# Kernel tuning notes

Measured on AMD Instinct MI355X. Metric: run time of the kernel, lower is better.

The kernel has to match this reference:

```python
import jax, jax.numpy as jnp
import numpy as np

B, N, H, NH, P = 32, 400, 512, 8, 3
DK = H // NH
SCALE = DK ** -0.5
EPS = 1e-5


def _ln(x, g, b):
    m = jnp.mean(x, axis=-1, keepdims=True)
    v = jnp.mean((x - m) ** 2, axis=-1, keepdims=True)
    return (x - m) * jax.lax.rsqrt(v + EPS) * g + b


def _split(x):  # [B,N,H] -> [B,h,N,dk]
    return x.reshape(x.shape[0], x.shape[1], NH, DK).transpose(0, 2, 1, 3)


def _merge(x):  # [B,h,N,dk] -> [B,N,H]
    return x.transpose(0, 2, 1, 3).reshape(x.shape[0], x.shape[2], H)


def _attn(q, k, v, mask):
    s = jnp.einsum('bhid,bhjd->bhij', q, k) * SCALE
    s = s * (1.0 + mask[:, None])  # learned multiplicative prior mask
    p = jax.nn.softmax(s, axis=-1)
    return jnp.einsum('bhij,bhjd->bhid', p, v)


def _weight_gen(pri, z, C, wq, keys, wf, bf):
    # pooled token query attends over the num_priors prior matrices
    qv = jnp.mean(z @ wq, axis=1)  # [B,H]
    aw = jax.nn.softmax((qv @ keys.T) * (H ** -0.5), axis=-1)  # [B,P]
    w = jnp.einsum('bp,bpij->bij', aw, pri)  # [B,N,N] fused prior mask
    fused = jnp.einsum('bij,bjh->bih', C, z) @ wf + bf  # [B,N,H] neighborhood fusion
    return w, aw, fused


def _ffn(x, w1, b1, w2, b2):
    return jax.nn.gelu(x @ w1 + b1, approximate=False) @ w2 + b2


def _forward(x_FC, x_SC, pri_FC, pri_SC, FC, SC, dw,
             ln_attn_FC_g, ln_attn_FC_b, ln_attn_SC_g, ln_attn_SC_b,
             ln_ffn_FC_g, ln_ffn_FC_b, ln_ffn_SC_g, ln_ffn_SC_b,
             qkv_FC_w, qkv_SC_w,
             ffn_FC_w1, ffn_FC_b1, ffn_FC_w2, ffn_FC_b2,
             ffn_SC_w1, ffn_SC_b1, ffn_SC_w2, ffn_SC_b2,
             wg_q_w, wg_keys, wg_fuse_w, wg_fuse_b,
             dist_in_FC_w, dist_in_FC_b, dist_in_SC_w, dist_in_SC_b,
             dist_out_FC_w, dist_out_FC_b, dist_out_SC_w, dist_out_SC_b):
    z_FC = _ln(x_FC, ln_attn_FC_g, ln_attn_FC_b)
    z_SC = _ln(x_SC, ln_attn_SC_g, ln_attn_SC_b)
    q_FC, k_FC, v_FC = [_split(t) for t in jnp.split(z_FC @ qkv_FC_w, 3, axis=-1)]
    q_SC, k_SC, v_SC = [_split(t) for t in jnp.split(z_SC @ qkv_SC_w, 3, axis=-1)]
    w_FC, aw_FC, fused_FC = _weight_gen(pri_FC, z_FC, FC, wg_q_w, wg_keys, wg_fuse_w, wg_fuse_b)
    w_SC, aw_SC, fused_SC = _weight_gen(pri_SC, z_SC, SC, wg_q_w, wg_keys, wg_fuse_w, wg_fuse_b)
    ctx_FC = _merge(_attn(q_FC, k_FC, v_FC, w_FC))
    ctx_SC = _merge(_attn(q_SC, k_SC, v_SC, w_SC))
    attn_out_FC = x_FC + ctx_FC + fused_FC
    attn_out_SC = x_SC + ctx_SC + fused_SC
    x_FC_new = attn_out_FC + _ffn(_ln(attn_out_FC, ln_ffn_FC_g, ln_ffn_FC_b), ffn_FC_w1, ffn_FC_b1, ffn_FC_w2, ffn_FC_b2)
    x_SC_new = attn_out_SC + _ffn(_ln(attn_out_SC, ln_ffn_SC_g, ln_ffn_SC_b), ffn_SC_w1, ffn_SC_b1, ffn_SC_w2, ffn_SC_b2)
    wf, ws = dw[0], dw[1]
    proj_FC = x_FC_new @ dist_in_FC_w + dist_in_FC_b
    proj_SC = x_SC_new @ dist_in_SC_w + dist_in_SC_b
    l_FC = jax.nn.log_softmax(proj_FC.reshape(-1, H), axis=-1)
    l_SC = jax.nn.log_softmax(proj_SC.reshape(-1, H), axis=-1)
    p_FC = jnp.exp(l_FC)
    p_SC = jnp.exp(l_SC)
    rows = jnp.float32(l_FC.shape[0])
    kl_FC = jnp.sum(p_SC * (l_SC - l_FC)) / rows  # KLDiv(batchmean)(l_FC, p_SC)
    kl_SC = jnp.sum(p_FC * (l_FC - l_SC)) / rows
    x_FC_out = (1.0 - wf) * x_FC_new + wf * (proj_FC @ dist_out_FC_w + dist_out_FC_b)
    x_SC_out = (1.0 - ws) * x_SC_new + ws * (proj_SC @ dist_out_SC_w + dist_out_SC_b)
    distill_loss = 0.5 * (kl_FC * wf + kl_SC * ws)
    return (x_FC_out, x_SC_out, distill_loss, aw_FC, aw_SC)


def setup_inputs() -> dict:
    key = jax.random.key(0)
    ks = jax.random.split(key, 24)
    init = lambda k, shape: 0.02 * jax.random.normal(k, shape, jnp.float32)
    d = {}
    d['x_FC'] = jax.random.normal(ks[0], (B, N, H), jnp.float32)
    d['x_SC'] = jax.random.normal(ks[1], (B, N, H), jnp.float32)
    d['pri_FC'] = jax.random.uniform(ks[2], (B, P, N, N), jnp.float32)
    d['pri_SC'] = jax.random.uniform(ks[3], (B, P, N, N), jnp.float32)
    d['FC'] = jax.random.uniform(ks[4], (B, N, N), jnp.float32)
    d['SC'] = jax.random.uniform(ks[5], (B, N, N), jnp.float32)
    d['dw'] = jnp.array([0.5, 0.5], jnp.float32)
    for nm in ['ln_attn_FC', 'ln_attn_SC', 'ln_ffn_FC', 'ln_ffn_SC']:
        d[nm + '_g'] = jnp.ones((H,), jnp.float32)
        d[nm + '_b'] = jnp.zeros((H,), jnp.float32)
    d['qkv_FC_w'] = init(ks[6], (H, 3 * H))
    d['qkv_SC_w'] = init(ks[7], (H, 3 * H))
    d['ffn_FC_w1'] = init(ks[8], (H, 4 * H)); d['ffn_FC_b1'] = jnp.zeros((4 * H,), jnp.float32)
    d['ffn_FC_w2'] = init(ks[9], (4 * H, H)); d['ffn_FC_b2'] = jnp.zeros((H,), jnp.float32)
    d['ffn_SC_w1'] = init(ks[10], (H, 4 * H)); d['ffn_SC_b1'] = jnp.zeros((4 * H,), jnp.float32)
    d['ffn_SC_w2'] = init(ks[11], (4 * H, H)); d['ffn_SC_b2'] = jnp.zeros((H,), jnp.float32)
    d['wg_q_w'] = init(ks[12], (H, H))
    d['wg_keys'] = init(ks[13], (P, H))
    d['wg_fuse_w'] = init(ks[14], (H, H)); d['wg_fuse_b'] = jnp.zeros((H,), jnp.float32)
    d['dist_in_FC_w'] = init(ks[15], (H, H)); d['dist_in_FC_b'] = jnp.zeros((H,), jnp.float32)
    d['dist_in_SC_w'] = init(ks[16], (H, H)); d['dist_in_SC_b'] = jnp.zeros((H,), jnp.float32)
    d['dist_out_FC_w'] = init(ks[17], (H, H)); d['dist_out_FC_b'] = jnp.zeros((H,), jnp.float32)
    d['dist_out_SC_w'] = init(ks[18], (H, H)); d['dist_out_SC_b'] = jnp.zeros((H,), jnp.float32)
    return d


def reference(x_FC, x_SC, pri_FC, pri_SC, FC, SC, dw,
              ln_attn_FC_g, ln_attn_FC_b, ln_attn_SC_g, ln_attn_SC_b,
              ln_ffn_FC_g, ln_ffn_FC_b, ln_ffn_SC_g, ln_ffn_SC_b,
              qkv_FC_w, qkv_SC_w,
              ffn_FC_w1, ffn_FC_b1, ffn_FC_w2, ffn_FC_b2,
              ffn_SC_w1, ffn_SC_b1, ffn_SC_w2, ffn_SC_b2,
              wg_q_w, wg_keys, wg_fuse_w, wg_fuse_b,
              dist_in_FC_w, dist_in_FC_b, dist_in_SC_w, dist_in_SC_b,
              dist_out_FC_w, dist_out_FC_b, dist_out_SC_w, dist_out_SC_b):
    return _forward(x_FC, x_SC, pri_FC, pri_SC, FC, SC, dw,
                    ln_attn_FC_g, ln_attn_FC_b, ln_attn_SC_g, ln_attn_SC_b,
                    ln_ffn_FC_g, ln_ffn_FC_b, ln_ffn_SC_g, ln_ffn_SC_b,
                    qkv_FC_w, qkv_SC_w,
                    ffn_FC_w1, ffn_FC_b1, ffn_FC_w2, ffn_FC_b2,
                    ffn_SC_w1, ffn_SC_b1, ffn_SC_w2, ffn_SC_b2,
                    wg_q_w, wg_keys, wg_fuse_w, wg_fuse_b,
                    dist_in_FC_w, dist_in_FC_b, dist_in_SC_w, dist_in_SC_b,
                    dist_out_FC_w, dist_out_FC_b, dist_out_SC_w, dist_out_SC_b)
```

## Files before the change

kernel.cpp:

```cpp
#include <hip/hip_runtime.h>
#include <hip/hip_bf16.h>
#include <math.h>

typedef __hip_bfloat16 bf16;

#define B_  32
#define N_  400
#define H_  512
#define NH_ 8
#define DK_ 64
#define P_  3
#define BN_ (B_*N_)
#define H3_ 1536
#define H4_ 2048

#define GLD16(g, l) __builtin_amdgcn_global_load_lds( \
    (__attribute__((address_space(1))) void*)(g), \
    (__attribute__((address_space(3))) void*)(l), 16, 0, 0)

__device__ __forceinline__ float b2f(bf16 v){ return __bfloat162float(v); }
__device__ __forceinline__ bf16  f2b(float v){ return __float2bfloat16(v); }
__device__ __forceinline__ float bfu(unsigned short u){ return __uint_as_float(((unsigned int)u)<<16); }
__device__ __forceinline__ unsigned short f2bu(float v){
  union { bf16 b; unsigned short u; } cv; cv.b = __float2bfloat16(v); return cv.u;
}
__device__ __forceinline__ bool is_f32(const void* gref){
  return *(const unsigned int*)gref == 0x3F800000u;
}
__device__ __forceinline__ float ldRaw(const void* p, long i, bool f32){
  return f32 ? ((const float*)p)[i] : b2f(((const bf16*)p)[i]);
}
__device__ __forceinline__ void stRaw(void* p, long i, float v, bool f32){
  if (f32) ((float*)p)[i] = v; else ((bf16*)p)[i] = f2b(v);
}

__device__ __forceinline__ float waveSum(float v){
  #pragma unroll
  for (int o=32;o>0;o>>=1) v += __shfl_xor(v,o,64);
  return v;
}
__device__ __forceinline__ float waveMax(float v){
  #pragma unroll
  for (int o=32;o>0;o>>=1) v = fmaxf(v,__shfl_xor(v,o,64));
  return v;
}
__device__ __forceinline__ float blockSum(float v, float* wred){
  v = waveSum(v);
  int w = threadIdx.x>>6, l = threadIdx.x&63;
  if (l==0) wred[w]=v;
  __syncthreads();
  float r = wred[0]+wred[1]+wred[2]+wred[3];
  __syncthreads();
  return r;
}
__device__ __forceinline__ float blockMax(float v, float* wred){
  v = waveMax(v);
  int w = threadIdx.x>>6, l = threadIdx.x&63;
  if (l==0) wred[w]=v;
  __syncthreads();
  float r = fmaxf(fmaxf(wred[0],wred[1]),fmaxf(wred[2],wred[3]));
  __syncthreads();
  return r;
}

template<int XMODE>
__global__ __launch_bounds__(256)
void ln_kernel(const void* __restrict__ x, const void* __restrict__ g,
               const void* __restrict__ bb, bf16* __restrict__ out,
               const void* __restrict__ gref)
{
  __shared__ float wred[4];
  const bool F32 = is_f32(gref);
  long row = blockIdx.x;
  int t = threadIdx.x;
  long base = row*H_;
  float v0, v1;
  if (XMODE==0){ v0 = ldRaw(x, base+t, F32); v1 = ldRaw(x, base+t+256, F32); }
  else         { v0 = b2f(((const bf16*)x)[base+t]); v1 = b2f(((const bf16*)x)[base+t+256]); }
  float mean = blockSum(v0+v1, wred) * (1.f/512.f);
  float d0 = v0-mean, d1 = v1-mean;
  float var = blockSum(d0*d0+d1*d1, wred) * (1.f/512.f);
  float rs = rsqrtf(var + 1e-5f);
  bf16* orow = out + base;
  orow[t]     = f2b(d0*rs*ldRaw(g,t,F32)     + ldRaw(bb,t,F32));
  orow[t+256] = f2b(d1*rs*ldRaw(g,t+256,F32) + ldRaw(bb,t+256,F32));
}

__global__ __launch_bounds__(256)
void tconv_kernel(const float* __restrict__ W, bf16* __restrict__ WT, int K, int N)
{
  __shared__ float tile[32][33];
  int n0 = blockIdx.x*32, k0 = blockIdx.y*32;
  int t = threadIdx.x;
  int c = t & 31, r = t >> 5;
  #pragma unroll
  for (int p=0;p<4;++p){
    int k = r + p*8;
    tile[k][c] = W[(long)(k0+k)*N + n0 + c];
  }
  __syncthreads();
  #pragma unroll
  for (int p=0;p<4;++p){
    int nn = r + p*8;
    WT[(long)(n0+nn)*K + k0 + c] = f2b(tile[c][nn]);
  }
}

__global__ __launch_bounds__(256)
void ztrans_kernel(const bf16* __restrict__ ZB, bf16* __restrict__ ZBT)
{
  __shared__ unsigned short tile[32][33];
  int j0 = blockIdx.x*32, h0 = blockIdx.y*32, b = blockIdx.z;
  int t = threadIdx.x;
  int c = t & 31, r = t >> 5;
  const unsigned short* src = (const unsigned short*)(ZB + (long)b*N_*H_);
  #pragma unroll
  for (int p=0;p<4;++p){
    int j = j0 + r + p*8;
    unsigned short v = 0;
    if (j < 400) v = src[(long)j*H_ + h0 + c];
    tile[r+p*8][c] = v;
  }
  __syncthreads();
  unsigned short* dst = (unsigned short*)(ZBT + (long)b*512*416);
  #pragma unroll
  for (int p=0;p<4;++p){
    int hh = r + p*8;
    dst[(long)(h0+hh)*416 + j0 + c] = tile[c][hh];
  }
}

__global__ __launch_bounds__(256)
void vtrans_kernel(const bf16* __restrict__ qkv, bf16* __restrict__ vtg)
{
  __shared__ unsigned short tile[32][33];
  int j0 = blockIdx.x*32, d0 = blockIdx.y*32, bh = blockIdx.z;
  int b = bh >> 3, h = bh & 7;
  int t = threadIdx.x;
  int c = t & 31, r = t >> 5;
  const unsigned short* src = (const unsigned short*)(qkv + (long)b*N_*H3_ + 1024 + h*64 + d0);
  #pragma unroll
  for (int p=0;p<4;++p){
    int j = j0 + r + p*8;
    unsigned short v = 0;
    if (j < 400) v = src[(long)j*H3_ + c];
    tile[r+p*8][c] = v;
  }
  __syncthreads();
  unsigned short* dst = (unsigned short*)(vtg + (long)bh*64*416);
  #pragma unroll
  for (int p=0;p<4;++p){
    int dd = r + p*8;
    dst[(long)(d0+dd)*416 + j0 + c] = tile[c][dd];
  }
}

template<int MI,int AMODE,int ACT,int RES,int OMODE>
__global__ __launch_bounds__(256)
void mgemm_kernel(const void* __restrict__ A, const bf16* __restrict__ BT,
                  const float* __restrict__ bias, const bf16* __restrict__ res,
                  void* __restrict__ out, long oOff,
                  int M, int Kl, int Kr, int Nn,
                  long sA, long sW, long sO,
                  const float* __restrict__ dwp, int dwidx)
{
  typedef __attribute__((ext_vector_type(8))) short bf16x8;
  typedef __attribute__((ext_vector_type(4))) float f32x4;
  constexpr int BM = MI*32;
  __shared__ unsigned short As[2][BM*32];
  __shared__ unsigned short Bs[2][128*32];
  int t = threadIdx.x;
  int w = t >> 6, l = t & 63;
  int wm = (w >> 1)*(MI*16), wn = (w & 1)*64;
  int m0 = blockIdx.y*BM, n0 = blockIdx.x*128;
  long zA = (long)blockIdx.z*sA;
  const bf16* Bb = BT + (long)blockIdx.z*sW;
  long zO = (long)blockIdx.z*sO;
  f32x4 acc[MI][4] = {};
  int lrow = l & 15, lkc = l >> 4;
  int srow = t >> 2, skc = t & 3;
  int nk = Kl >> 5;
  int buf = 0;

  if (AMODE==0){
    #pragma unroll
    for (int half=0; half<MI/2; ++half){
      const unsigned short* gA = (const unsigned short*)A + zA + (long)(m0+srow+half*64)*Kr + skc*8;
      GLD16(gA, &As[0][w*512 + half*2048]);
    }
    #pragma unroll
    for (int half=0; half<2; ++half){
      const unsigned short* gB = (const unsigned short*)Bb + (long)(n0+srow+half*64)*Kl + skc*8;
      GLD16(gB, &Bs[0][w*512 + half*2048]);
    }
    __syncthreads();
    for (int kt=0; kt<nk; ++kt){
      if (kt+1 < nk){
        int k1 = (kt+1) << 5;
        #pragma unroll
        for (int half=0; half<MI/2; ++half){
          const unsigned short* gA = (const unsigned short*)A + zA + (long)(m0+srow+half*64)*Kr + k1 + skc*8;
          GLD16(gA, &As[buf^1][w*512 + half*2048]);
        }
        #pragma unroll
        for (int half=0; half<2; ++half){
          const unsigned short* gB = (const unsigned short*)Bb + (long)(n0+srow+half*64)*Kl + k1 + skc*8;
          GLD16(gB, &Bs[buf^1][w*512 + half*2048]);
        }
      }
      bf16x8 af[MI], bf_[4];
      #pragma unroll
      for (int i=0;i<MI;++i) af[i]  = *(const bf16x8*)&As[buf][(wm + i*16 + lrow)*32 + lkc*8];
      #pragma unroll
      for (int i=0;i<4;++i)  bf_[i] = *(const bf16x8*)&Bs[buf][(wn + i*16 + lrow)*32 + lkc*8];
      #pragma unroll
      for (int mi=0;mi<MI;++mi)
        #pragma unroll
        for (int ni=0;ni<4;++ni)
          acc[mi][ni] = __builtin_amdgcn_mfma_f32_16x16x32_bf16(bf_[ni], af[mi], acc[mi][ni], 0, 0, 0);
      __syncthreads();
      buf ^= 1;
    }
  } else {
    for (int kt=0; kt<nk; ++kt){
      int k0 = kt << 5;
      #pragma unroll
      for (int half=0; half<MI/2; ++half){
        int row = srow + half*64;
        int gm = m0 + row;
        int gk = k0 + skc*8;
        uint4 va = make_uint4(0,0,0,0);
        if (gm < M && gk < Kr){
          const float* ap = (const float*)A + zA + (long)gm*Kr + gk;
          float4 f0 = *(const float4*)ap;
          float4 f1 = *(const float4*)(ap+4);
          union { uint4 u; unsigned short s[8]; } pv;
          pv.s[0]=f2bu(f0.x); pv.s[1]=f2bu(f0.y); pv.s[2]=f2bu(f0.z); pv.s[3]=f2bu(f0.w);
          pv.s[4]=f2bu(f1.x); pv.s[5]=f2bu(f1.y); pv.s[6]=f2bu(f1.z); pv.s[7]=f2bu(f1.w);
          va = pv.u;
        }
        *(uint4*)&As[0][row*32 + skc*8] = va;
      }
      #pragma unroll
      for (int half=0; half<2; ++half){
        int row = srow + half*64;
        uint4 vb = *(const uint4*)((const unsigned short*)Bb + (long)(n0+row)*Kl + k0 + skc*8);
        *(uint4*)&Bs[0][row*32 + skc*8] = vb;
      }
      __syncthreads();
      bf16x8 af[MI], bf_[4];
      #pragma unroll
      for (int i=0;i<MI;++i) af[i]  = *(const bf16x8*)&As[0][(wm + i*16 + lrow)*32 + lkc*8];
      #pragma unroll
      for (int i=0;i<4;++i)  bf_[i] = *(const bf16x8*)&Bs[0][(wn + i*16 + lrow)*32 + lkc*8];
      #pragma unroll
      for (int mi=0;mi<MI;++mi)
        #pragma unroll
        for (int ni=0;ni<4;++ni)
          acc[mi][ni] = __builtin_amdgcn_mfma_f32_16x16x32_bf16(bf_[ni], af[mi], acc[mi][ni], 0, 0, 0);
      __syncthreads();
    }
  }
  float wbl = (RES==2) ? dwp[dwidx] : 0.f;
  #pragma unroll
  for (int mi=0;mi<MI;++mi){
    int gm = m0 + wm + mi*16 + lrow;
    if (gm >= M) continue;
    #pragma unroll
    for (int ni=0;ni<4;++ni){
      int gnb = n0 + wn + ni*16 + lkc*4;
      long o = zO + (long)gm*Nn + gnb;
      float v0 = acc[mi][ni][0], v1 = acc[mi][ni][1], v2 = acc[mi][ni][2], v3 = acc[mi][ni][3];
      if (bias){
        float4 bv = *(const float4*)&bias[gnb];
        v0 += bv.x; v1 += bv.y; v2 += bv.z; v3 += bv.w;
      }
      if (ACT==1){
        v0 = 0.5f*v0*(1.f + erff(v0*0.70710678118654752f));
        v1 = 0.5f*v1*(1.f + erff(v1*0.70710678118654752f));
        v2 = 0.5f*v2*(1.f + erff(v2*0.70710678118654752f));
        v3 = 0.5f*v3*(1.f + erff(v3*0.70710678118654752f));
      }
      if (RES==1){
        ushort4 r4 = *(const ushort4*)((const unsigned short*)res + o);
        v0 += bfu(r4.x); v1 += bfu(r4.y); v2 += bfu(r4.z); v3 += bfu(r4.w);
      }
      if (RES==2){
        ushort4 r4 = *(const ushort4*)((const unsigned short*)res + o);
        v0 = (1.f-wbl)*bfu(r4.x) + wbl*v0;
        v1 = (1.f-wbl)*bfu(r4.y) + wbl*v1;
        v2 = (1.f-wbl)*bfu(r4.z) + wbl*v2;
        v3 = (1.f-wbl)*bfu(r4.w) + wbl*v3;
      }
      if (OMODE==0){
        ushort4 o4;
        o4.x = f2bu(v0); o4.y = f2bu(v1); o4.z = f2bu(v2); o4.w = f2bu(v3);
        *(ushort4*)((unsigned short*)out + o) = o4;
      } else {
        *(float4*)((float*)out + oOff + o) = make_float4(v0,v1,v2,v3);
      }
    }
  }
}

__global__ __launch_bounds__(256)
void zbar_kernel(const bf16* __restrict__ Z, float* __restrict__ zbar)
{
  __shared__ float red[256];
  int hc = blockIdx.x, b = blockIdx.y;
  int t = threadIdx.x;
  int col = hc*64 + (t & 63), ns = t >> 6;
  const bf16* p = Z + (long)b*N_*H_ + (long)ns*100*H_ + col;
  float s = 0.f;
  for (int n=0;n<100;++n) s += b2f(p[(long)n*H_]);
  red[t] = s;
  __syncthreads();
  if (t < 64){
    float tot = red[t]+red[t+64]+red[t+128]+red[t+192];
    zbar[b*512 + hc*64 + t] = tot * (1.f/400.f);
  }
}

__global__ __launch_bounds__(256)
void qv_kernel(const float* __restrict__ zbar, const void* __restrict__ wq,
               float* __restrict__ qv, const void* __restrict__ gref)
{
  __shared__ float red[256];
  const bool F32 = is_f32(gref);
  int ch = blockIdx.x, b = blockIdx.y;
  int t = threadIdx.x;
  int col = ch*32 + (t & 31), ks = t >> 5;
  const float* zb = zbar + b*512;
  float s = 0.f;
  int k0 = ks*64;
  for (int k=0;k<64;++k)
    s = fmaf(zb[k0+k], ldRaw(wq, (long)(k0+k)*512 + col, F32), s);
  red[t] = s;
  __syncthreads();
  if (t < 32){
    float q = 0.f;
    #pragma unroll
    for (int i=0;i<8;++i) q += red[t + i*32];
    qv[b*512 + ch*32 + t] = q;
  }
}

__global__ __launch_bounds__(256)
void aw_kernel(const float* __restrict__ qv, const void* __restrict__ keys,
               float* __restrict__ awf, void* __restrict__ outbase, long offAw,
               const void* __restrict__ gref)
{
  __shared__ float wred[4];
  const bool F32 = is_f32(gref);
  int b = blockIdx.x, t = threadIdx.x;
  const float* q = qv + b*512;
  float lg[3];
  #pragma unroll
  for (int p=0;p<3;++p){
    float part = q[t]*ldRaw(keys, p*512+t, F32) + q[t+256]*ldRaw(keys, p*512+t+256, F32);
    lg[p] = blockSum(part, wred) * 0.04419417382415922f;
  }
  float m = fmaxf(lg[0], fmaxf(lg[1], lg[2]));
  float e0 = expf(lg[0]-m), e1 = expf(lg[1]-m), e2 = expf(lg[2]-m);
  float inv = 1.f/(e0+e1+e2);
  if (t<3){
    float a = (t==0?e0:(t==1?e1:e2))*inv;
    awf[b*3+t] = a;
    stRaw(outbase, offAw + b*3 + t, a, F32);
  }
}

__global__ __launch_bounds__(256)
void wcomb_kernel(const void* __restrict__ pri, const float* __restrict__ awf,
                  bf16* __restrict__ WM, const void* __restrict__ gref)
{
  const bool F32 = is_f32(gref);
  long u = (long)blockIdx.x*256 + threadIdx.x;
  long e0 = u*4;
  int b = (int)(e0 / 160000);
  long r = e0 - (long)b*160000;
  float a0 = awf[b*3+0], a1 = awf[b*3+1], a2 = awf[b*3+2];
  float o0,o1,o2,o3;
  if (F32){
    const float* p0 = (const float*)pri + (long)b*3*160000 + r;
    float4 a = *(const float4*)(p0);
    float4 c = *(const float4*)(p0 + 160000);
    float4 d = *(const float4*)(p0 + 320000);
    o0 = a0*a.x + a1*c.x + a2*d.x;
    o1 = a0*a.y + a1*c.y + a2*d.y;
    o2 = a0*a.z + a1*c.z + a2*d.z;
    o3 = a0*a.w + a1*c.w + a2*d.w;
  } else {
    const bf16* p0 = (const bf16*)pri + (long)b*3*160000 + r;
    ushort4 a = *(const ushort4*)(p0);
    ushort4 c = *(const ushort4*)(p0 + 160000);
    ushort4 d = *(const ushort4*)(p0 + 320000);
    o0 = a0*bfu(a.x) + a1*bfu(c.x) + a2*bfu(d.x);
    o1 = a0*bfu(a.y) + a1*bfu(c.y) + a2*bfu(d.y);
    o2 = a0*bfu(a.z) + a1*bfu(c.z) + a2*bfu(d.z);
    o3 = a0*bfu(a.w) + a1*bfu(c.w) + a2*bfu(d.w);
  }
  ushort4 o;
  o.x = f2bu(o0); o.y = f2bu(o1); o.z = f2bu(o2); o.w = f2bu(o3);
  *(ushort4*)(WM + e0) = o;
}

__global__ __launch_bounds__(64)
void attn_kernel(const bf16* __restrict__ qkv, const bf16* __restrict__ wm,
                 const bf16* __restrict__ vtg, const void* __restrict__ x,
                 const bf16* __restrict__ fused, bf16* __restrict__ aout,
                 const void* __restrict__ gref)
{
  typedef __attribute__((ext_vector_type(8))) short bf16x8;
  typedef __attribute__((ext_vector_type(4))) float f32x4;
  __shared__ unsigned short Pbuf[2][16*40];
  const bool F32 = is_f32(gref);
  int h = blockIdx.x, b = blockIdx.y, qt = blockIdx.z;
  int l = threadIdx.x;
  int lr = l & 15, lg = l >> 4;
  int i0 = qt*16;
  const bf16* qb = qkv + (long)b*N_*H3_ + h*64;
  const bf16* kb = qb + 512;
  const bf16* wrow = wm + (long)b*N_*N_;
  const bf16* vt = vtg + (long)(b*NH_ + h)*64*416;
  bf16x8 qf0 = *(const bf16x8*)(qb + (long)(i0+lr)*H3_ + lg*8);
  bf16x8 qf1 = *(const bf16x8*)(qb + (long)(i0+lr)*H3_ + 32 + lg*8);
  float rm = -1e30f, rl = 0.f;
  f32x4 o[4] = {};
  #pragma unroll
  for (int w=0; w<13; ++w){
    int t0 = 2*w, t1 = 2*w+1;
    f32x4 s0, s1;
    {
      bf16x8 kf0 = *(const bf16x8*)(kb + (long)(t0*16+lr)*H3_ + lg*8);
      bf16x8 kf1 = *(const bf16x8*)(kb + (long)(t0*16+lr)*H3_ + 32 + lg*8);
      f32x4 st = {0.f,0.f,0.f,0.f};
      st = __builtin_amdgcn_mfma_f32_16x16x32_bf16(kf0, qf0, st, 0,0,0);
      st = __builtin_amdgcn_mfma_f32_16x16x32_bf16(kf1, qf1, st, 0,0,0);
      uint2 w4 = *(const uint2*)(wrow + (long)(i0+lr)*400 + t0*16 + lg*4);
      s0[0] = st[0]*0.125f*(1.f + bfu((unsigned short)(w4.x & 0xffffu)));
      s0[1] = st[1]*0.125f*(1.f + bfu((unsigned short)(w4.x >> 16)));
      s0[2] = st[2]*0.125f*(1.f + bfu((unsigned short)(w4.y & 0xffffu)));
      s0[3] = st[3]*0.125f*(1.f + bfu((unsigned short)(w4.y >> 16)));
    }
    if (t1 < 25){
      bf16x8 kf0 = *(const bf16x8*)(kb + (long)(t1*16+lr)*H3_ + lg*8);
      bf16x8 kf1 = *(const bf16x8*)(kb + (long)(t1*16+lr)*H3_ + 32 + lg*8);
      f32x4 st = {0.f,0.f,0.f,0.f};
      st = __builtin_amdgcn_mfma_f32_16x16x32_bf16(kf0, qf0, st, 0,0,0);
      st = __builtin_amdgcn_mfma_f32_16x16x32_bf16(kf1, qf1, st, 0,0,0);
      uint2 w4 = *(const uint2*)(wrow + (long)(i0+lr)*400 + t1*16 + lg*4);
      s1[0] = st[0]*0.125f*(1.f + bfu((unsigned short)(w4.x & 0xffffu)));
      s1[1] = st[1]*0.125f*(1.f + bfu((unsigned short)(w4.x >> 16)));
      s1[2] = st[2]*0.125f*(1.f + bfu((unsigned short)(w4.y & 0xffffu)));
      s1[3] = st[3]*0.125f*(1.f + bfu((unsigned short)(w4.y >> 16)));
    } else {
      s1[0]=s1[1]=s1[2]=s1[3] = -1e30f;
    }
    float tm = fmaxf(fmaxf(fmaxf(s0[0],s0[1]), fmaxf(s0[2],s0[3])),
                     fmaxf(fmaxf(s1[0],s1[1]), fmaxf(s1[2],s1[3])));
    tm = fmaxf(tm, __shfl_xor(tm, 16));
    tm = fmaxf(tm, __shfl_xor(tm, 32));
    float mn = fmaxf(rm, tm);
    float sc = expf(rm - mn);
    unsigned pk0x, pk0y, pk1x = 0u, pk1y = 0u;
    float ls = 0.f;
    {
      unsigned u0 = f2bu(expf(s0[0]-mn)), u1 = f2bu(expf(s0[1]-mn));
      unsigned u2 = f2bu(expf(s0[2]-mn)), u3 = f2bu(expf(s0[3]-mn));
      pk0x = u0 | (u1<<16); pk0y = u2 | (u3<<16);
      ls += __uint_as_float(u0<<16) + __uint_as_float(u1<<16)
          + __uint_as_float(u2<<16) + __uint_as_float(u3<<16);
    }
    if (t1 < 25){
      unsigned u0 = f2bu(expf(s1[0]-mn)), u1 = f2bu(expf(s1[1]-mn));
      unsigned u2 = f2bu(expf(s1[2]-mn)), u3 = f2bu(expf(s1[3]-mn));
      pk1x = u0 | (u1<<16); pk1y = u2 | (u3<<16);
      ls += __uint_as_float(u0<<16) + __uint_as_float(u1<<16)
          + __uint_as_float(u2<<16) + __uint_as_float(u3<<16);
    }
    ls += __shfl_xor(ls, 16);
    ls += __shfl_xor(ls, 32);
    rl = rl*sc + ls;
    rm = mn;
    unsigned short* pb = Pbuf[w & 1];
    *(uint2*)&pb[lr*40 + lg*4]      = make_uint2(pk0x, pk0y);
    *(uint2*)&pb[lr*40 + 16 + lg*4] = make_uint2(pk1x, pk1y);
    bf16x8 pa = *(const bf16x8*)&pb[lr*40 + lg*8];
    float sq0 = __shfl(sc, lg*4 + 0);
    float sq1 = __shfl(sc, lg*4 + 1);
    float sq2 = __shfl(sc, lg*4 + 2);
    float sq3 = __shfl(sc, lg*4 + 3);
    #pragma unroll
    for (int dt=0; dt<4; ++dt){
      o[dt][0] *= sq0; o[dt][1] *= sq1; o[dt][2] *= sq2; o[dt][3] *= sq3;
      bf16x8 vf = *(const bf16x8*)(vt + (long)(dt*16+lr)*416 + w*32 + lg*8);
      o[dt] = __builtin_amdgcn_mfma_f32_16x16x32_bf16(pa, vf, o[dt], 0,0,0);
    }
  }
  float invl = 1.f/rl;
  #pragma unroll
  for (int q=0;q<4;++q){
    float iv = __shfl(invl, lg*4 + q);
    long gi = (long)(b*N_ + i0 + lg*4 + q);
    #pragma unroll
    for (int dt=0;dt<4;++dt){
      long oi = gi*H_ + h*64 + dt*16 + lr;
      float xv = F32 ? ((const float*)x)[oi] : b2f(((const bf16*)x)[oi]);
      float fv = b2f(fused[oi]);
      aout[oi] = f2b(o[dt][q]*iv + xv + fv);
    }
  }
}

__global__ __launch_bounds__(256)
void kl_rows_kernel(const bf16* __restrict__ pF, const bf16* __restrict__ pS,
                    float2* __restrict__ rowpart)
{
  __shared__ float wred[4];
  long row = blockIdx.x;
  int t = threadIdx.x;
  const bf16* fr = pF + row*512;
  const bf16* sr = pS + row*512;
  float f0 = b2f(fr[t]), f1 = b2f(fr[t+256]), s0 = b2f(sr[t]), s1 = b2f(sr[t+256]);
  float mF = blockMax(fmaxf(f0,f1), wred);
  float mS = blockMax(fmaxf(s0,s1), wred);
  float sumF = blockSum(expf(f0-mF)+expf(f1-mF), wred);
  float sumS = blockSum(expf(s0-mS)+expf(s1-mS), wred);
  float lseF = mF + logf(sumF), lseS = mS + logf(sumS);
  float lF0 = f0-lseF, lF1 = f1-lseF, lS0 = s0-lseS, lS1 = s1-lseS;
  float pS0 = expf(lS0), pS1 = expf(lS1), pF0 = expf(lF0), pF1 = expf(lF1);
  float a  = pS0*(lS0-lF0) + pS1*(lS1-lF1);
  float bb = pF0*(lF0-lS0) + pF1*(lF1-lS1);
  a  = blockSum(a,  wred);
  bb = blockSum(bb, wred);
  if (t==0) rowpart[row] = make_float2(a, bb);
}

__global__ __launch_bounds__(256)
void kl_final_kernel(const float2* __restrict__ rowpart, const void* __restrict__ dw,
                     void* __restrict__ outbase, long offLoss,
                     const void* __restrict__ gref)
{
  __shared__ float wred[4];
  const bool F32 = is_f32(gref);
  int t = threadIdx.x;
  float sa=0.f, sb=0.f;
  for (int i=t;i<BN_;i+=256){ float2 v = rowpart[i]; sa+=v.x; sb+=v.y; }
  sa = blockSum(sa, wred);
  sb = blockSum(sb, wred);
  if (t==0){
    float wf = ldRaw(dw,0,F32), ws = ldRaw(dw,1,F32);
    float loss = 0.5f*((sa/12800.f)*wf + (sb/12800.f)*ws);
    stRaw(outbase, offLoss, loss, F32);
  }
}

#define OFF_ZB    0L
#define OFF_QKV   13107200L
#define OFF_FUSED 52428800L
#define OFF_WM    65536000L
#define OFF_CZ    75776000L
#define OFF_PROJ0 88883200L
#define OFF_PROJ1 101990400L
#define OFF_QKVT  115097600L
#define OFF_W1T   116670464L
#define OFF_W2T   118767616L
#define OFF_FUT   120864768L
#define OFF_DIT   121389056L
#define OFF_DOT   121913344L
#define OFF_ZBT   122437632L
#define OFF_ZBAR  136069120L
#define OFF_AWF   136134656L
#define OFF_ROWP  136135680L
#define OFF_VTG   136238080L
#define OFF_QV    149869568L

extern "C" void kernel_launch(void* const* d_in, const int* in_sizes, int n_in,
                              void* d_out, int out_size, void* d_ws, size_t ws_size,
                              hipStream_t stream)
{
  (void)in_sizes; (void)n_in; (void)out_size; (void)ws_size;
  const void* x[2]    = {d_in[0],  d_in[1]};
  const void* pri[2]  = {d_in[2],  d_in[3]};
  const float* Cm[2]  = {(const float*)d_in[4], (const float*)d_in[5]};
  const float* dwf    =  (const float*)d_in[6];
  const void* lnag[2] = {d_in[7],  d_in[9]};
  const void* lnab[2] = {d_in[8],  d_in[10]};
  const void* lnfg[2] = {d_in[11], d_in[13]};
  const void* lnfb[2] = {d_in[12], d_in[14]};
  const float* qkvw[2]= {(const float*)d_in[15], (const float*)d_in[16]};
  const float* fw1[2] = {(const float*)d_in[17], (const float*)d_in[21]};
  const float* fb1[2] = {(const float*)d_in[18], (const float*)d_in[22]};
  const float* fw2[2] = {(const float*)d_in[19], (const float*)d_in[23]};
  const float* fb2[2] = {(const float*)d_in[20], (const float*)d_in[24]};
  const void* wgq     =  d_in[25];
  const void* wgk     =  d_in[26];
  const float* wgfw   =  (const float*)d_in[27];
  const float* wgfb   =  (const float*)d_in[28];
  const float* diw[2] = {(const float*)d_in[29], (const float*)d_in[31]};
  const float* dib[2] = {(const float*)d_in[30], (const float*)d_in[32]};
  const float* dow[2] = {(const float*)d_in[33], (const float*)d_in[35]};
  const float* dob[2] = {(const float*)d_in[34], (const float*)d_in[36]};
  const void* gref    =  d_in[7];

  char* ws = (char*)d_ws;
  bf16*  ZB    = (bf16*)(ws + OFF_ZB);
  bf16*  LN2   = (bf16*)(ws + OFF_ZB);
  bf16*  XNEW  = (bf16*)(ws + OFF_ZB);
  bf16*  QKV   = (bf16*)(ws + OFF_QKV);
  bf16*  HH    = (bf16*)(ws + OFF_QKV);
  bf16*  FUSED = (bf16*)(ws + OFF_FUSED);
  bf16*  WM    = (bf16*)(ws + OFF_WM);
  bf16*  CZ    = (bf16*)(ws + OFF_CZ);
  bf16*  AOUT  = (bf16*)(ws + OFF_CZ);
  bf16*  PROJ[2] = {(bf16*)(ws + OFF_PROJ0), (bf16*)(ws + OFF_PROJ1)};
  bf16*  QKVT  = (bf16*)(ws + OFF_QKVT);
  bf16*  W1T   = (bf16*)(ws + OFF_W1T);
  bf16*  W2T   = (bf16*)(ws + OFF_W2T);
  bf16*  FUT   = (bf16*)(ws + OFF_FUT);
  bf16*  DIT   = (bf16*)(ws + OFF_DIT);
  bf16*  DOT   = (bf16*)(ws + OFF_DOT);
  bf16*  ZBT   = (bf16*)(ws + OFF_ZBT);
  bf16*  VTG   = (bf16*)(ws + OFF_VTG);
  float* ZBAR  = (float*)(ws + OFF_ZBAR);
  float* AWF   = (float*)(ws + OFF_AWF);
  float2* ROWP = (float2*)(ws + OFF_ROWP);
  float* QV    = (float*)(ws + OFF_QV);

  const long offX[2]  = {0L, 6553600L};
  const long offLoss  = 13107200L;
  const long offAw[2] = {13107201L, 13107297L};

  for (int s=0; s<2; ++s){
    tconv_kernel<<<dim3(48,16),256,0,stream>>>(qkvw[s], QKVT, 512, 1536);
    tconv_kernel<<<dim3(64,16),256,0,stream>>>(fw1[s],  W1T,  512, 2048);
    tconv_kernel<<<dim3(16,64),256,0,stream>>>(fw2[s],  W2T,  2048, 512);
    tconv_kernel<<<dim3(16,16),256,0,stream>>>(wgfw,    FUT,  512, 512);
    tconv_kernel<<<dim3(16,16),256,0,stream>>>(diw[s],  DIT,  512, 512);
    tconv_kernel<<<dim3(16,16),256,0,stream>>>(dow[s],  DOT,  512, 512);
    ln_kernel<0><<<BN_,256,0,stream>>>(x[s], lnag[s], lnab[s], ZB, gref);
    zbar_kernel<<<dim3(8,B_),256,0,stream>>>(ZB, ZBAR);
    ztrans_kernel<<<dim3(13,16,32),256,0,stream>>>(ZB, ZBT);
    mgemm_kernel<4,0,0,0,0><<<dim3(12,100,1),256,0,stream>>>(
        ZB, QKVT, nullptr, nullptr, QKV, 0, BN_, 512, 512, H3_, 0,0,0, nullptr,0);
    vtrans_kernel<<<dim3(13,2,256),256,0,stream>>>(QKV, VTG);
    qv_kernel<<<dim3(16,B_),256,0,stream>>>(ZBAR, wgq, QV, gref);
    aw_kernel<<<B_,256,0,stream>>>(QV, wgk, AWF, d_out, offAw[s], gref);
    wcomb_kernel<<<5000,256,0,stream>>>(pri[s], AWF, WM, gref);
    mgemm_kernel<4,1,0,0,0><<<dim3(4,4,32),256,0,stream>>>(
        Cm[s], ZBT, nullptr, nullptr, CZ, 0, 400, 416, 400, 512,
        160000L, 212992L, 204800L, nullptr,0);
    mgemm_kernel<2,0,0,0,0><<<dim3(4,200,1),256,0,stream>>>(
        CZ, FUT, wgfb, nullptr, FUSED, 0, BN_, 512, 512, 512, 0,0,0, nullptr,0);
    attn_kernel<<<dim3(NH_,B_,25),64,0,stream>>>(QKV, WM, VTG, x[s], FUSED, AOUT, gref);
    ln_kernel<1><<<BN_,256,0,stream>>>(AOUT, lnfg[s], lnfb[s], LN2, gref);
    mgemm_kernel<4,0,1,0,0><<<dim3(16,100,1),256,0,stream>>>(
        LN2, W1T, fb1[s], nullptr, HH, 0, BN_, 512, 512, H4_, 0,0,0, nullptr,0);
    mgemm_kernel<2,0,0,1,0><<<dim3(4,200,1),256,0,stream>>>(
        HH, W2T, fb2[s], AOUT, XNEW, 0, BN_, 2048, 2048, 512, 0,0,0, nullptr,0);
    mgemm_kernel<2,0,0,0,0><<<dim3(4,200,1),256,0,stream>>>(
        XNEW, DIT, dib[s], nullptr, PROJ[s], 0, BN_, 512, 512, 512, 0,0,0, nullptr,0);
    mgemm_kernel<2,0,0,2,1><<<dim3(4,200,1),256,0,stream>>>(
        PROJ[s], DOT, dob[s], XNEW, d_out, offX[s], BN_, 512, 512, 512, 0,0,0, dwf, s);
  }
  kl_rows_kernel<<<BN_,256,0,stream>>>(PROJ[0], PROJ[1], ROWP);
  kl_final_kernel<<<1,256,0,stream>>>(ROWP, dwf, d_out, offLoss, gref);
}
```

Baseline: 1.001 ms.

## Batch weight transposes into one launch, pre-convert C to bf16, use fast exp

Six per-weight transpose/convert launches become one kernel that picks its segment from the block index, which cuts launch overhead. The fp32 neighbourhood matrix C is converted to padded bf16 in a separate pass, so the C·Z GEMM can take the plain bf16 A path instead of converting fp32 on the fly. The CB buffer aliases the VTG workspace, so the V transpose moves to after that GEMM. The attention softmax and KL kernels switch from expf/logf to the fast __expf/__logf intrinsics, at slightly lower accuracy.

```diff
diff --git a/kernel.cpp b/kernel.cpp
--- a/kernel.cpp
+++ b/kernel.cpp
@@ -86,22 +86,36 @@
   orow[t+256] = f2b(d1*rs*ldRaw(g,t+256,F32) + ldRaw(bb,t+256,F32));
 }
 
-__global__ __launch_bounds__(256)
-void tconv_kernel(const float* __restrict__ W, bf16* __restrict__ WT, int K, int N)
+struct TC6 {
+  const float* W[6];
+  bf16* WT[6];
+  int K[6]; int N[6]; int base[6];
+};
+__global__ __launch_bounds__(256)
+void tc6_kernel(TC6 p)
 {
   __shared__ float tile[32][33];
-  int n0 = blockIdx.x*32, k0 = blockIdx.y*32;
+  int gt = blockIdx.x;
+  int seg = 0;
+  #pragma unroll
+  for (int i=1;i<6;++i) if (gt >= p.base[i]) seg = i;
+  int lt = gt - p.base[seg];
+  int K = p.K[seg], N = p.N[seg];
+  int ntx = N >> 5;
+  int n0 = (lt % ntx)*32, k0 = (lt / ntx)*32;
+  const float* W = p.W[seg];
+  bf16* WT = p.WT[seg];
   int t = threadIdx.x;
   int c = t & 31, r = t >> 5;
   #pragma unroll
-  for (int p=0;p<4;++p){
-    int k = r + p*8;
+  for (int q=0;q<4;++q){
+    int k = r + q*8;
     tile[k][c] = W[(long)(k0+k)*N + n0 + c];
   }
   __syncthreads();
   #pragma unroll
-  for (int p=0;p<4;++p){
-    int nn = r + p*8;
+  for (int q=0;q<4;++q){
+    int nn = r + q*8;
     WT[(long)(n0+nn)*K + k0 + c] = f2b(tile[c][nn]);
   }
 }
@@ -128,6 +142,25 @@
     int hh = r + p*8;
     dst[(long)(h0+hh)*416 + j0 + c] = tile[c][hh];
   }
+}
+
+__global__ __launch_bounds__(256)
+void cconv_kernel(const float* __restrict__ C, bf16* __restrict__ CB)
+{
+  long u = ((long)blockIdx.x*256 + threadIdx.x)*8;
+  int b = (int)(u / (512*416));
+  int rem = (int)(u - (long)b*(512*416));
+  int r = rem / 416, c = rem % 416;
+  ushort4 lo = {0,0,0,0}, hi = {0,0,0,0};
+  if (r < 400 && c < 400){
+    const float* p = C + (long)b*160000 + r*400 + c;
+    float4 f0 = *(const float4*)p;
+    float4 f1 = *(const float4*)(p+4);
+    lo.x=f2bu(f0.x); lo.y=f2bu(f0.y); lo.z=f2bu(f0.z); lo.w=f2bu(f0.w);
+    hi.x=f2bu(f1.x); hi.y=f2bu(f1.y); hi.z=f2bu(f1.z); hi.w=f2bu(f1.w);
+  }
+  *(ushort4*)((unsigned short*)CB + u)     = lo;
+  *(ushort4*)((unsigned short*)CB + u + 4) = hi;
 }
 
 __global__ __launch_bounds__(256)
@@ -462,19 +495,19 @@
     tm = fmaxf(tm, __shfl_xor(tm, 16));
     tm = fmaxf(tm, __shfl_xor(tm, 32));
     float mn = fmaxf(rm, tm);
-    float sc = expf(rm - mn);
+    float sc = __expf(rm - mn);
     unsigned pk0x, pk0y, pk1x = 0u, pk1y = 0u;
     float ls = 0.f;
     {
-      unsigned u0 = f2bu(expf(s0[0]-mn)), u1 = f2bu(expf(s0[1]-mn));
-      unsigned u2 = f2bu(expf(s0[2]-mn)), u3 = f2bu(expf(s0[3]-mn));
+      unsigned u0 = f2bu(__expf(s0[0]-mn)), u1 = f2bu(__expf(s0[1]-mn));
+      unsigned u2 = f2bu(__expf(s0[2]-mn)), u3 = f2bu(__expf(s0[3]-mn));
       pk0x = u0 | (u1<<16); pk0y = u2 | (u3<<16);
       ls += __uint_as_float(u0<<16) + __uint_as_float(u1<<16)
           + __uint_as_float(u2<<16) + __uint_as_float(u3<<16);
     }
     if (t1 < 25){
-      unsigned u0 = f2bu(expf(s1[0]-mn)), u1 = f2bu(expf(s1[1]-mn));
-      unsigned u2 = f2bu(expf(s1[2]-mn)), u3 = f2bu(expf(s1[3]-mn));
+      unsigned u0 = f2bu(__expf(s1[0]-mn)), u1 = f2bu(__expf(s1[1]-mn));
+      unsigned u2 = f2bu(__expf(s1[2]-mn)), u3 = f2bu(__expf(s1[3]-mn));
       pk1x = u0 | (u1<<16); pk1y = u2 | (u3<<16);
       ls += __uint_as_float(u0<<16) + __uint_as_float(u1<<16)
           + __uint_as_float(u2<<16) + __uint_as_float(u3<<16);
@@ -525,11 +558,11 @@
   float f0 = b2f(fr[t]), f1 = b2f(fr[t+256]), s0 = b2f(sr[t]), s1 = b2f(sr[t+256]);
   float mF = blockMax(fmaxf(f0,f1), wred);
   float mS = blockMax(fmaxf(s0,s1), wred);
-  float sumF = blockSum(expf(f0-mF)+expf(f1-mF), wred);
-  float sumS = blockSum(expf(s0-mS)+expf(s1-mS), wred);
-  float lseF = mF + logf(sumF), lseS = mS + logf(sumS);
+  float sumF = blockSum(__expf(f0-mF)+__expf(f1-mF), wred);
+  float sumS = blockSum(__expf(s0-mS)+__expf(s1-mS), wred);
+  float lseF = mF + __logf(sumF), lseS = mS + __logf(sumS);
   float lF0 = f0-lseF, lF1 = f1-lseF, lS0 = s0-lseS, lS1 = s1-lseS;
-  float pS0 = expf(lS0), pS1 = expf(lS1), pF0 = expf(lF0), pF1 = expf(lF1);
+  float pS0 = __expf(lS0), pS1 = __expf(lS1), pF0 = __expf(lF0), pF1 = __expf(lF1);
   float a  = pS0*(lS0-lF0) + pS1*(lS1-lF1);
   float bb = pF0*(lF0-lS0) + pF1*(lF1-lS1);
   a  = blockSum(a,  wred);
@@ -623,6 +656,7 @@
   bf16*  DOT   = (bf16*)(ws + OFF_DOT);
   bf16*  ZBT   = (bf16*)(ws + OFF_ZBT);
   bf16*  VTG   = (bf16*)(ws + OFF_VTG);
+  bf16*  CB    = (bf16*)(ws + OFF_VTG);
   float* ZBAR  = (float*)(ws + OFF_ZBAR);
   float* AWF   = (float*)(ws + OFF_AWF);
   float2* ROWP = (float2*)(ws + OFF_ROWP);
@@ -633,26 +667,31 @@
   const long offAw[2] = {13107201L, 13107297L};
 
   for (int s=0; s<2; ++s){
-    tconv_kernel<<<dim3(48,16),256,0,stream>>>(qkvw[s], QKVT, 512, 1536);
-    tconv_kernel<<<dim3(64,16),256,0,stream>>>(fw1[s],  W1T,  512, 2048);
-    tconv_kernel<<<dim3(16,64),256,0,stream>>>(fw2[s],  W2T,  2048, 512);
-    tconv_kernel<<<dim3(16,16),256,0,stream>>>(wgfw,    FUT,  512, 512);
-    tconv_kernel<<<dim3(16,16),256,0,stream>>>(diw[s],  DIT,  512, 512);
-    tconv_kernel<<<dim3(16,16),256,0,stream>>>(dow[s],  DOT,  512, 512);
+    TC6 tp;
+    tp.W[0]=qkvw[s]; tp.WT[0]=QKVT; tp.K[0]=512;  tp.N[0]=1536;
+    tp.W[1]=fw1[s];  tp.WT[1]=W1T;  tp.K[1]=512;  tp.N[1]=2048;
+    tp.W[2]=fw2[s];  tp.WT[2]=W2T;  tp.K[2]=2048; tp.N[2]=512;
+    tp.W[3]=wgfw;    tp.WT[3]=FUT;  tp.K[3]=512;  tp.N[3]=512;
+    tp.W[4]=diw[s];  tp.WT[4]=DIT;  tp.K[4]=512;  tp.N[4]=512;
+    tp.W[5]=dow[s];  tp.WT[5]=DOT;  tp.K[5]=512;  tp.N[5]=512;
+    tp.base[0]=0; tp.base[1]=768; tp.base[2]=1792; tp.base[3]=2816;
+    tp.base[4]=3072; tp.base[5]=3328;
+    tc6_kernel<<<3584,256,0,stream>>>(tp);
     ln_kernel<0><<<BN_,256,0,stream>>>(x[s], lnag[s], lnab[s], ZB, gref);
     zbar_kernel<<<dim3(8,B_),256,0,stream>>>(ZB, ZBAR);
     ztrans_kernel<<<dim3(13,16,32),256,0,stream>>>(ZB, ZBT);
+    cconv_kernel<<<3328,256,0,stream>>>(Cm[s], CB);
     mgemm_kernel<4,0,0,0,0><<<dim3(12,100,1),256,0,stream>>>(
         ZB, QKVT, nullptr, nullptr, QKV, 0, BN_, 512, 512, H3_, 0,0,0, nullptr,0);
-    vtrans_kernel<<<dim3(13,2,256),256,0,stream>>>(QKV, VTG);
     qv_kernel<<<dim3(16,B_),256,0,stream>>>(ZBAR, wgq, QV, gref);
     aw_kernel<<<B_,256,0,stream>>>(QV, wgk, AWF, d_out, offAw[s], gref);
     wcomb_kernel<<<5000,256,0,stream>>>(pri[s], AWF, WM, gref);
-    mgemm_kernel<4,1,0,0,0><<<dim3(4,4,32),256,0,stream>>>(
-        Cm[s], ZBT, nullptr, nullptr, CZ, 0, 400, 416, 400, 512,
-        160000L, 212992L, 204800L, nullptr,0);
+    mgemm_kernel<4,0,0,0,0><<<dim3(4,4,32),256,0,stream>>>(
+        CB, ZBT, nullptr, nullptr, CZ, 0, 400, 416, 416, 512,
+        212992L, 212992L, 204800L, nullptr,0);
     mgemm_kernel<2,0,0,0,0><<<dim3(4,200,1),256,0,stream>>>(
         CZ, FUT, wgfb, nullptr, FUSED, 0, BN_, 512, 512, 512, 0,0,0, nullptr,0);
+    vtrans_kernel<<<dim3(13,2,256),256,0,stream>>>(QKV, VTG);
     attn_kernel<<<dim3(NH_,B_,25),64,0,stream>>>(QKV, WM, VTG, x[s], FUSED, AOUT, gref);
     ln_kernel<1><<<BN_,256,0,stream>>>(AOUT, lnfg[s], lnfb[s], LN2, gref);
     mgemm_kernel<4,0,1,0,0><<<dim3(16,100,1),256,0,stream>>>(
```

Result: faster. 912.2 us (-8.9%).
